# Kernel tuning notes

Measured on AMD Instinct MI355X. Metric: run time of the kernel, lower is better.

## Reference

```python
import jax, jax.numpy as jnp
import numpy as np

N_NODES = 50000
N_EDGES = 1600000
IN_FEATS = 256
NUM_HEADS = 4
OUT_FEATS = 32
NEG_SLOPE = 0.2


def setup_inputs() -> dict:
    key = jax.random.key(0)
    k_feat, k_src, k_dst, k_w, k_al, k_ar = jax.random.split(key, 6)
    feat = jax.random.normal(k_feat, (N_NODES, IN_FEATS), dtype=jnp.float32)
    src = jax.random.randint(k_src, (N_EDGES,), 0, N_NODES, dtype=jnp.int32)
    dst = jax.random.randint(k_dst, (N_EDGES,), 0, N_NODES, dtype=jnp.int32)
    # Glorot/xavier-like scales
    w_scale = np.sqrt(2.0 / (IN_FEATS + NUM_HEADS * OUT_FEATS)).astype(np.float32)
    a_scale = np.sqrt(2.0 / (1 + OUT_FEATS)).astype(np.float32)
    W_fc = jax.random.normal(k_w, (NUM_HEADS * OUT_FEATS, IN_FEATS), dtype=jnp.float32) * w_scale
    attn_l = jax.random.normal(k_al, (1, NUM_HEADS, OUT_FEATS), dtype=jnp.float32) * a_scale
    attn_r = jax.random.normal(k_ar, (1, NUM_HEADS, OUT_FEATS), dtype=jnp.float32) * a_scale
    bias = jnp.zeros((NUM_HEADS * OUT_FEATS,), dtype=jnp.float32)
    return {"feat": feat, "W_fc": W_fc, "attn_l": attn_l, "attn_r": attn_r,
            "bias": bias, "src": src, "dst": dst}


def reference(feat, W_fc, attn_l, attn_r, bias, src, dst):
    N = feat.shape[0]
    H, F = NUM_HEADS, OUT_FEATS
    # dense projection: [N, H, F]
    h = (feat @ W_fc.T).reshape(N, H, F)
    # per-node attention logits: [N, H]
    el = (h * attn_l).sum(axis=-1)
    er = (h * attn_r).sum(axis=-1)
    # u_add_v edge score + leaky relu: [E, H]
    e = el[src] + er[dst]
    e = jnp.where(e >= 0, e, NEG_SLOPE * e)
    # segment softmax over destination nodes
    m = jax.ops.segment_max(e, dst, num_segments=N)          # [N, H]
    m = jnp.where(jnp.isfinite(m), m, 0.0)                   # guard 0-in-degree
    e_exp = jnp.exp(e - m[dst])                              # [E, H]
    denom = jax.ops.segment_sum(e_exp, dst, num_segments=N)  # [N, H]
    denom = jnp.where(denom > 0, denom, 1.0)
    a = e_exp / denom[dst]                                   # [E, H]
    # weighted message aggregation: [N, H, F]
    msg = h[src] * a[:, :, None]                             # [E, H, F]
    out = jax.ops.segment_sum(msg, dst, num_segments=N)
    out = out + bias.reshape(1, H, F)
    return out
```

## Files before the change

kernel.cpp:

```cpp
#include <hip/hip_runtime.h>

typedef __attribute__((ext_vector_type(8))) short bf16x8;
typedef __attribute__((ext_vector_type(4))) float f32x4;

#define IN_F 256
#define HF 128
#define NHEADS 4
#define NEG 0.2f
#define GBM 128
#define GBK 64
#define LDK 72

#define RB 256
#define NBP 200
#define CHUNK 6400
#define ITPT 25
#define BCAP 10000

#define FUSED_SMEM (GBM * LDK * 2 * 2)

__device__ __forceinline__ unsigned short f2bf(float x) {
    unsigned u = __float_as_uint(x);
    unsigned r = (u + 0x7FFFu + ((u >> 16) & 1u)) >> 16;
    return (unsigned short)r;
}
__device__ __forceinline__ float bf2f(unsigned short b) {
    return __uint_as_float((unsigned)b << 16);
}

__global__ __launch_bounds__(256) void fused1_kernel(
    const float* __restrict__ feat, const float* __restrict__ W,
    const float* __restrict__ al, const float* __restrict__ ar,
    unsigned short* __restrict__ hb, float* __restrict__ el, float* __restrict__ er,
    const int* __restrict__ src, const int* __restrict__ dst,
    int* __restrict__ ebuf, int* __restrict__ cntArr, int* __restrict__ ofsArr,
    int N, int E, int GG)
{
    extern __shared__ char smem[];
    const int t = threadIdx.x;

    if ((int)blockIdx.x < GG) {
        unsigned short (*As)[LDK] = (unsigned short(*)[LDK])smem;
        unsigned short (*Bs)[LDK] = (unsigned short(*)[LDK])(smem + GBM * LDK * 2);
        const int n0 = blockIdx.x * GBM;
        const int lane = t & 63;
        const int wid = t >> 6;
        const int wm = (wid >> 1) * 64;
        const int wn = (wid & 1) * 64;
        const int lr = lane & 15;
        const int lk = (lane >> 4) * 8;

        f32x4 acc[4][4];
#pragma unroll
        for (int i = 0; i < 4; i++)
#pragma unroll
            for (int j = 0; j < 4; j++) acc[i][j] = (f32x4){0.f, 0.f, 0.f, 0.f};

        for (int k0 = 0; k0 < IN_F; k0 += GBK) {
#pragma unroll
            for (int r = 0; r < 4; r++) {
                int idx = t + r * 256;
                int row = idx >> 3;
                int c8 = (idx & 7) * 8;
                int n = n0 + row;
                float4 v0 = make_float4(0.f, 0.f, 0.f, 0.f), v1 = v0;
                if (n < N) {
                    v0 = *(const float4*)&feat[(size_t)n * IN_F + k0 + c8];
                    v1 = *(const float4*)&feat[(size_t)n * IN_F + k0 + c8 + 4];
                }
                bf16x8 sa;
                sa[0] = f2bf(v0.x); sa[1] = f2bf(v0.y); sa[2] = f2bf(v0.z); sa[3] = f2bf(v0.w);
                sa[4] = f2bf(v1.x); sa[5] = f2bf(v1.y); sa[6] = f2bf(v1.z); sa[7] = f2bf(v1.w);
                *(bf16x8*)&As[row][c8] = sa;
                float4 w0 = *(const float4*)&W[(size_t)row * IN_F + k0 + c8];
                float4 w1 = *(const float4*)&W[(size_t)row * IN_F + k0 + c8 + 4];
                bf16x8 sb;
                sb[0] = f2bf(w0.x); sb[1] = f2bf(w0.y); sb[2] = f2bf(w0.z); sb[3] = f2bf(w0.w);
                sb[4] = f2bf(w1.x); sb[5] = f2bf(w1.y); sb[6] = f2bf(w1.z); sb[7] = f2bf(w1.w);
                *(bf16x8*)&Bs[row][c8] = sb;
            }
            __syncthreads();
#pragma unroll
            for (int ks = 0; ks < 2; ks++) {
                bf16x8 a[4], b[4];
#pragma unroll
                for (int mi = 0; mi < 4; mi++) a[mi] = *(bf16x8*)&As[wm + mi * 16 + lr][ks * 32 + lk];
#pragma unroll
                for (int ni = 0; ni < 4; ni++) b[ni] = *(bf16x8*)&Bs[wn + ni * 16 + lr][ks * 32 + lk];
#pragma unroll
                for (int mi = 0; mi < 4; mi++)
#pragma unroll
                    for (int ni = 0; ni < 4; ni++)
                        acc[mi][ni] = __builtin_amdgcn_mfma_f32_16x16x32_bf16(a[mi], b[ni], acc[mi][ni], 0, 0, 0);
            }
            __syncthreads();
        }
        const int crow = (lane >> 4) * 4;
#pragma unroll
        for (int mi = 0; mi < 4; mi++)
#pragma unroll
            for (int j = 0; j < 4; j++) {
                int n = n0 + wm + mi * 16 + crow + j;
                if (n < N) {
#pragma unroll
                    for (int ni = 0; ni < 4; ni++) {
                        int o = wn + ni * 16 + lr;
                        hb[(size_t)n * HF + o] = f2bf(acc[mi][ni][j]);
                    }
                }
            }
        float al_c[4], ar_c[4];
#pragma unroll
        for (int ni = 0; ni < 4; ni++) {
            int o = wn + ni * 16 + lr;
            al_c[ni] = al[o];
            ar_c[ni] = ar[o];
        }
        float* elp = (float*)smem;
        float* erp = elp + 128 * 4;
        const int h0 = wn >> 5;
#pragma unroll
        for (int mi = 0; mi < 4; mi++)
#pragma unroll
            for (int j = 0; j < 4; j++) {
                float e0 = acc[mi][0][j] * al_c[0] + acc[mi][1][j] * al_c[1];
                float e1 = acc[mi][2][j] * al_c[2] + acc[mi][3][j] * al_c[3];
                float r0 = acc[mi][0][j] * ar_c[0] + acc[mi][1][j] * ar_c[1];
                float r1 = acc[mi][2][j] * ar_c[2] + acc[mi][3][j] * ar_c[3];
#pragma unroll
                for (int off = 1; off < 16; off <<= 1) {
                    e0 += __shfl_xor(e0, off);
                    e1 += __shfl_xor(e1, off);
                    r0 += __shfl_xor(r0, off);
                    r1 += __shfl_xor(r1, off);
                }
                if (lr == 0) {
                    int row = wm + mi * 16 + crow + j;
                    elp[row * 4 + h0]     = e0;
                    elp[row * 4 + h0 + 1] = e1;
                    erp[row * 4 + h0]     = r0;
                    erp[row * 4 + h0 + 1] = r1;
                }
            }
        __syncthreads();
        if (t < 128) {
            int n = n0 + t;
            if (n < N) {
                *(float4*)&el[(size_t)n * 4] = *(float4*)&elp[t * 4];
                *(float4*)&er[(size_t)n * 4] = *(float4*)&erp[t * 4];
            }
        }
    } else {
        int* cnt = (int*)smem;
        int* sc  = cnt + 256;
        int* cur = sc + 256;
        int* stage = cur + 256;
        const int blk = blockIdx.x - GG;
        const int eb = blk * CHUNK;
        cnt[t] = 0;
        __syncthreads();

        int bkt[ITPT], ent[ITPT];
#pragma unroll
        for (int i = 0; i < ITPT; i++) {
            int idx = eb + i * 256 + t;
            int b = NBP - 1, e = 0;
            if (idx < E) {
                int d = dst[idx];
                int s = src[idx];
                b = d >> 8;
                e = s | ((d & 255) << 24);
            }
            bkt[i] = b;
            ent[i] = e;
            atomicAdd(&cnt[b], 1);
        }
        __syncthreads();
        int orig = cnt[t];
        sc[t] = orig;
        __syncthreads();
        for (int off = 1; off < 256; off <<= 1) {
            int v = (t >= off) ? sc[t - off] : 0;
            __syncthreads();
            sc[t] += v;
            __syncthreads();
        }
        int excl = sc[t] - orig;
        if (t < NBP) {
            cntArr[blk * NBP + t] = orig;
            ofsArr[blk * NBP + t] = excl;
        }
        cur[t] = excl;
        __syncthreads();
#pragma unroll
        for (int i = 0; i < ITPT; i++) {
            int pos = atomicAdd(&cur[bkt[i]], 1);
            stage[pos] = ent[i];
        }
        __syncthreads();
#pragma unroll
        for (int i = 0; i < ITPT; i++) {
            int idx = i * 256 + t;
            ebuf[eb + idx] = stage[idx];
        }
    }
}

__global__ __launch_bounds__(256) void bscan_kernel(const int* __restrict__ cntArr,
                                                    int* __restrict__ bucketStart, int nblk) {
    __shared__ int sums[256];
    const int t = threadIdx.x;
    int s = 0;
    if (t < NBP)
        for (int blk = 0; blk < nblk; blk++) s += cntArr[blk * NBP + t];
    sums[t] = s;
    __syncthreads();
    for (int off = 1; off < 256; off <<= 1) {
        int v = (t >= off) ? sums[t - off] : 0;
        __syncthreads();
        sums[t] += v;
        __syncthreads();
    }
    if (t < NBP) bucketStart[t] = sums[t] - s;
}

__global__ __launch_bounds__(256) void bsort_kernel(const int* __restrict__ ebuf,
                                                    const int* __restrict__ cntArr,
                                                    const int* __restrict__ ofsArr,
                                                    const int* __restrict__ bucketStart,
                                                    int* __restrict__ rowStart,
                                                    int* __restrict__ esrc,
                                                    int nblk, int N, int E) {
    __shared__ int lcnt[256];
    __shared__ int lsc[256];
    __shared__ int lcur[256];
    __shared__ int sorted[BCAP];
    const int b = blockIdx.x, t = threadIdx.x;
    const int gbase = bucketStart[b];
    lcnt[t] = 0;
    __syncthreads();

    int rbase = 0, rlen = 0;
    if (t < nblk) {
        rbase = t * CHUNK + ofsArr[t * NBP + b];
        rlen = cntArr[t * NBP + b];
    }
    int i = 0;
    for (; i + 3 < rlen; i += 4) {
        unsigned e0 = (unsigned)ebuf[rbase + i];
        unsigned e1 = (unsigned)ebuf[rbase + i + 1];
        unsigned e2 = (unsigned)ebuf[rbase + i + 2];
        unsigned e3 = (unsigned)ebuf[rbase + i + 3];
        atomicAdd(&lcnt[e0 >> 24], 1);
        atomicAdd(&lcnt[e1 >> 24], 1);
        atomicAdd(&lcnt[e2 >> 24], 1);
        atomicAdd(&lcnt[e3 >> 24], 1);
    }
    for (; i < rlen; i++) {
        unsigned e = (unsigned)ebuf[rbase + i];
        atomicAdd(&lcnt[e >> 24], 1);
    }
    __syncthreads();
    int orig = lcnt[t];
    lsc[t] = orig;
    __syncthreads();
    for (int off = 1; off < 256; off <<= 1) {
        int v = (t >= off) ? lsc[t - off] : 0;
        __syncthreads();
        lsc[t] += v;
        __syncthreads();
    }
    int excl = lsc[t] - orig;
    int node = b * RB + t;
    if (node < N) rowStart[node] = gbase + excl;
    if (b == 0 && t == 0) rowStart[N] = E;
    lcur[t] = excl;
    __syncthreads();
    i = 0;
    for (; i + 3 < rlen; i += 4) {
        unsigned e0 = (unsigned)ebuf[rbase + i];
        unsigned e1 = (unsigned)ebuf[rbase + i + 1];
        unsigned e2 = (unsigned)ebuf[rbase + i + 2];
        unsigned e3 = (unsigned)ebuf[rbase + i + 3];
        sorted[atomicAdd(&lcur[e0 >> 24], 1)] = (int)(e0 & 0xFFFFFFu);
        sorted[atomicAdd(&lcur[e1 >> 24], 1)] = (int)(e1 & 0xFFFFFFu);
        sorted[atomicAdd(&lcur[e2 >> 24], 1)] = (int)(e2 & 0xFFFFFFu);
        sorted[atomicAdd(&lcur[e3 >> 24], 1)] = (int)(e3 & 0xFFFFFFu);
    }
    for (; i < rlen; i++) {
        unsigned e = (unsigned)ebuf[rbase + i];
        sorted[atomicAdd(&lcur[e >> 24], 1)] = (int)(e & 0xFFFFFFu);
    }
    __syncthreads();
    const int total = lsc[255];
    for (int k = t; k < total; k += 256) esrc[gbase + k] = sorted[k];
}

__global__ __launch_bounds__(256) void agg_kernel(const int* __restrict__ rowStart,
                                                  const int* __restrict__ esrc,
                                                  const unsigned short* __restrict__ hb,
                                                  const float* __restrict__ el,
                                                  const float* __restrict__ er,
                                                  const float* __restrict__ bias,
                                                  float* __restrict__ out, int N) {
    const int wid = threadIdx.x >> 6;
    const int lane = threadIdx.x & 63;
    const int n = blockIdx.x * 4 + wid;
    if (n >= N) return;
    const int lg = lane & 15;
    const int grp = lane >> 4;
    const int head = lg >> 2;
    const float ern = er[n * NHEADS + head];
    const int beg = rowStart[n];
    const int end = rowStart[n + 1];

    float acc[8];
#pragma unroll
    for (int i = 0; i < 8; i++) acc[i] = 0.f;
    float den = 0.f;

#pragma unroll 2
    for (int j = beg + grp; j < end; j += 4) {
        int s = esrc[j];
        float x = el[s * NHEADS + head] + ern;
        x = x >= 0.f ? x : NEG * x;
        float sv = __expf(x);
        uint4 hv = *(const uint4*)&hb[(size_t)s * HF + lg * 8];
        acc[0] += sv * bf2f((unsigned short)(hv.x & 0xFFFFu));
        acc[1] += sv * bf2f((unsigned short)(hv.x >> 16));
        acc[2] += sv * bf2f((unsigned short)(hv.y & 0xFFFFu));
        acc[3] += sv * bf2f((unsigned short)(hv.y >> 16));
        acc[4] += sv * bf2f((unsigned short)(hv.z & 0xFFFFu));
        acc[5] += sv * bf2f((unsigned short)(hv.z >> 16));
        acc[6] += sv * bf2f((unsigned short)(hv.w & 0xFFFFu));
        acc[7] += sv * bf2f((unsigned short)(hv.w >> 16));
        den += sv;
    }

#pragma unroll
    for (int off = 16; off < 64; off <<= 1) {
#pragma unroll
        for (int i = 0; i < 8; i++) acc[i] += __shfl_xor(acc[i], off);
        den += __shfl_xor(den, off);
    }

    if (lane < 16) {
        float inv = 1.f / (den > 0.f ? den : 1.f);
        float4 b0 = *(const float4*)&bias[lg * 8];
        float4 b1 = *(const float4*)&bias[lg * 8 + 4];
        float4 o0, o1;
        o0.x = acc[0] * inv + b0.x; o0.y = acc[1] * inv + b0.y;
        o0.z = acc[2] * inv + b0.z; o0.w = acc[3] * inv + b0.w;
        o1.x = acc[4] * inv + b1.x; o1.y = acc[5] * inv + b1.y;
        o1.z = acc[6] * inv + b1.z; o1.w = acc[7] * inv + b1.w;
        *(float4*)&out[(size_t)n * HF + lg * 8] = o0;
        *(float4*)&out[(size_t)n * HF + lg * 8 + 4] = o1;
    }
}

extern "C" void kernel_launch(void* const* d_in, const int* in_sizes, int n_in,
                              void* d_out, int out_size, void* d_ws, size_t ws_size,
                              hipStream_t stream) {
    const float* feat = (const float*)d_in[0];
    const float* W    = (const float*)d_in[1];
    const float* al   = (const float*)d_in[2];
    const float* ar   = (const float*)d_in[3];
    const float* bias = (const float*)d_in[4];
    const int*   src  = (const int*)d_in[5];
    const int*   dst  = (const int*)d_in[6];
    const int N = in_sizes[0] / IN_F;
    const int E = in_sizes[5];
    float* out = (float*)d_out;

    const int nblk = (E + CHUNK - 1) / CHUNK;
    const int NBUCK = (N + RB - 1) / RB;
    const int GG = (N + GBM - 1) / GBM;

    unsigned short* hb = (unsigned short*)d_ws;
    float* el       = (float*)(hb + (size_t)N * HF);
    float* er       = el + (size_t)N * NHEADS;
    int* rowStart   = (int*)(er + (size_t)N * NHEADS);
    int* esrc       = rowStart + (N + 1);
    int* ebuf       = esrc + E;
    int* cntArr     = ebuf + (size_t)nblk * CHUNK;
    int* ofsArr     = cntArr + (size_t)nblk * NBP;
    int* bucketStart= ofsArr + (size_t)nblk * NBP;

    fused1_kernel<<<GG + nblk, 256, FUSED_SMEM, stream>>>(
        feat, W, al, ar, hb, el, er, src, dst, ebuf, cntArr, ofsArr, N, E, GG);
    bscan_kernel<<<1, 256, 0, stream>>>(cntArr, bucketStart, nblk);
    bsort_kernel<<<NBUCK, 256, 0, stream>>>(ebuf, cntArr, ofsArr, bucketStart,
                                            rowStart, esrc, nblk, N, E);
    agg_kernel<<<(N + 3) / 4, 256, 0, stream>>>(rowStart, esrc, hb, el, er, bias, out, N);
}
```

Measured before the change: 140.9 us.

## Pre-convert W to bf16 and compute GEMM directly from registers without LDS

Adds a small kernel that converts W to bf16 once per call. The projection GEMM then drops its LDS staging and barriers: each wave loads its 32 feature rows straight from global into MFMA operands and reads the bf16 W fragments from global/L2. Each wave now covers all 128 output columns, so el/er are reduced inside the wave and written directly. The cost is an extra launch and redundant W reads per wave, which rely on cache hits. The shared-memory size is also set from the partition branch's needs.

Measured after the change: 163.8 us. 1.16x slower.

```diff
diff --git a/kernel.cpp b/kernel.cpp
--- a/kernel.cpp
+++ b/kernel.cpp
@@ -7,9 +7,6 @@
 #define HF 128
 #define NHEADS 4
 #define NEG 0.2f
-#define GBM 128
-#define GBK 64
-#define LDK 72
 
 #define RB 256
 #define NBP 200
@@ -17,7 +14,7 @@
 #define ITPT 25
 #define BCAP 10000
 
-#define FUSED_SMEM (GBM * LDK * 2 * 2)
+#define PART_SMEM ((256 * 3 + CHUNK) * 4)
 
 __device__ __forceinline__ unsigned short f2bf(float x) {
     unsigned u = __float_as_uint(x);
@@ -27,9 +24,26 @@
 __device__ __forceinline__ float bf2f(unsigned short b) {
     return __uint_as_float((unsigned)b << 16);
 }
+__device__ __forceinline__ bf16x8 cvt8(float4 x, float4 y) {
+    bf16x8 r;
+    r[0] = f2bf(x.x); r[1] = f2bf(x.y); r[2] = f2bf(x.z); r[3] = f2bf(x.w);
+    r[4] = f2bf(y.x); r[5] = f2bf(y.y); r[6] = f2bf(y.z); r[7] = f2bf(y.w);
+    return r;
+}
+
+__global__ __launch_bounds__(256) void wconv_kernel(const float* __restrict__ W,
+                                                    unsigned short* __restrict__ Wb) {
+    int i = (blockIdx.x * 256 + threadIdx.x) * 4;
+    if (i < HF * IN_F) {
+        float4 v = *(const float4*)&W[i];
+        ushort4 o;
+        o.x = f2bf(v.x); o.y = f2bf(v.y); o.z = f2bf(v.z); o.w = f2bf(v.w);
+        *(ushort4*)&Wb[i] = o;
+    }
+}
 
 __global__ __launch_bounds__(256) void fused1_kernel(
-    const float* __restrict__ feat, const float* __restrict__ W,
+    const float* __restrict__ feat, const unsigned short* __restrict__ Wb,
     const float* __restrict__ al, const float* __restrict__ ar,
     unsigned short* __restrict__ hb, float* __restrict__ el, float* __restrict__ er,
     const int* __restrict__ src, const int* __restrict__ dst,
@@ -40,116 +54,84 @@
     const int t = threadIdx.x;
 
     if ((int)blockIdx.x < GG) {
-        unsigned short (*As)[LDK] = (unsigned short(*)[LDK])smem;
-        unsigned short (*Bs)[LDK] = (unsigned short(*)[LDK])(smem + GBM * LDK * 2);
-        const int n0 = blockIdx.x * GBM;
         const int lane = t & 63;
         const int wid = t >> 6;
-        const int wm = (wid >> 1) * 64;
-        const int wn = (wid & 1) * 64;
+        const int base = blockIdx.x * 128 + wid * 32;
         const int lr = lane & 15;
-        const int lk = (lane >> 4) * 8;
-
-        f32x4 acc[4][4];
-#pragma unroll
-        for (int i = 0; i < 4; i++)
-#pragma unroll
-            for (int j = 0; j < 4; j++) acc[i][j] = (f32x4){0.f, 0.f, 0.f, 0.f};
-
-        for (int k0 = 0; k0 < IN_F; k0 += GBK) {
-#pragma unroll
-            for (int r = 0; r < 4; r++) {
-                int idx = t + r * 256;
-                int row = idx >> 3;
-                int c8 = (idx & 7) * 8;
-                int n = n0 + row;
-                float4 v0 = make_float4(0.f, 0.f, 0.f, 0.f), v1 = v0;
+        const int lkO = (lane >> 4) * 8;
+
+        const int r0 = base + lr;
+        const int r1 = base + 16 + lr;
+        const bool v0 = r0 < N, v1 = r1 < N;
+        const float* arow0 = feat + (size_t)r0 * IN_F + lkO;
+        const float* arow1 = feat + (size_t)r1 * IN_F + lkO;
+
+        f32x4 acc[2][8];
+#pragma unroll
+        for (int mi = 0; mi < 2; mi++)
+#pragma unroll
+            for (int ni = 0; ni < 8; ni++) acc[mi][ni] = (f32x4){0.f, 0.f, 0.f, 0.f};
+
+        const float4 z4 = make_float4(0.f, 0.f, 0.f, 0.f);
+#pragma unroll
+        for (int ks = 0; ks < 8; ks++) {
+            const int k0 = ks * 32;
+            bf16x8 a0, a1;
+            {
+                float4 x0 = v0 ? *(const float4*)(arow0 + k0) : z4;
+                float4 x1 = v0 ? *(const float4*)(arow0 + k0 + 4) : z4;
+                a0 = cvt8(x0, x1);
+                float4 y0 = v1 ? *(const float4*)(arow1 + k0) : z4;
+                float4 y1 = v1 ? *(const float4*)(arow1 + k0 + 4) : z4;
+                a1 = cvt8(y0, y1);
+            }
+            bf16x8 b[8];
+#pragma unroll
+            for (int ni = 0; ni < 8; ni++)
+                b[ni] = *(const bf16x8*)&Wb[(size_t)(ni * 16 + lr) * IN_F + k0 + lkO];
+#pragma unroll
+            for (int ni = 0; ni < 8; ni++) {
+                acc[0][ni] = __builtin_amdgcn_mfma_f32_16x16x32_bf16(a0, b[ni], acc[0][ni], 0, 0, 0);
+                acc[1][ni] = __builtin_amdgcn_mfma_f32_16x16x32_bf16(a1, b[ni], acc[1][ni], 0, 0, 0);
+            }
+        }
+
+        float al_c[8], ar_c[8];
+#pragma unroll
+        for (int ni = 0; ni < 8; ni++) {
+            al_c[ni] = al[ni * 16 + lr];
+            ar_c[ni] = ar[ni * 16 + lr];
+        }
+        const int crow = (lane >> 4) * 4;
+#pragma unroll
+        for (int mi = 0; mi < 2; mi++)
+#pragma unroll
+            for (int j = 0; j < 4; j++) {
+                int n = base + mi * 16 + crow + j;
                 if (n < N) {
-                    v0 = *(const float4*)&feat[(size_t)n * IN_F + k0 + c8];
-                    v1 = *(const float4*)&feat[(size_t)n * IN_F + k0 + c8 + 4];
+#pragma unroll
+                    for (int ni = 0; ni < 8; ni++)
+                        hb[(size_t)n * HF + ni * 16 + lr] = f2bf(acc[mi][ni][j]);
                 }
-                bf16x8 sa;
-                sa[0] = f2bf(v0.x); sa[1] = f2bf(v0.y); sa[2] = f2bf(v0.z); sa[3] = f2bf(v0.w);
-                sa[4] = f2bf(v1.x); sa[5] = f2bf(v1.y); sa[6] = f2bf(v1.z); sa[7] = f2bf(v1.w);
-                *(bf16x8*)&As[row][c8] = sa;
-                float4 w0 = *(const float4*)&W[(size_t)row * IN_F + k0 + c8];
-                float4 w1 = *(const float4*)&W[(size_t)row * IN_F + k0 + c8 + 4];
-                bf16x8 sb;
-                sb[0] = f2bf(w0.x); sb[1] = f2bf(w0.y); sb[2] = f2bf(w0.z); sb[3] = f2bf(w0.w);
-                sb[4] = f2bf(w1.x); sb[5] = f2bf(w1.y); sb[6] = f2bf(w1.z); sb[7] = f2bf(w1.w);
-                *(bf16x8*)&Bs[row][c8] = sb;
-            }
-            __syncthreads();
-#pragma unroll
-            for (int ks = 0; ks < 2; ks++) {
-                bf16x8 a[4], b[4];
-#pragma unroll
-                for (int mi = 0; mi < 4; mi++) a[mi] = *(bf16x8*)&As[wm + mi * 16 + lr][ks * 32 + lk];
-#pragma unroll
-                for (int ni = 0; ni < 4; ni++) b[ni] = *(bf16x8*)&Bs[wn + ni * 16 + lr][ks * 32 + lk];
-#pragma unroll
-                for (int mi = 0; mi < 4; mi++)
-#pragma unroll
-                    for (int ni = 0; ni < 4; ni++)
-                        acc[mi][ni] = __builtin_amdgcn_mfma_f32_16x16x32_bf16(a[mi], b[ni], acc[mi][ni], 0, 0, 0);
-            }
-            __syncthreads();
-        }
-        const int crow = (lane >> 4) * 4;
-#pragma unroll
-        for (int mi = 0; mi < 4; mi++)
-#pragma unroll
-            for (int j = 0; j < 4; j++) {
-                int n = n0 + wm + mi * 16 + crow + j;
-                if (n < N) {
-#pragma unroll
-                    for (int ni = 0; ni < 4; ni++) {
-                        int o = wn + ni * 16 + lr;
-                        hb[(size_t)n * HF + o] = f2bf(acc[mi][ni][j]);
+                float e[4], r[4];
+#pragma unroll
+                for (int h = 0; h < 4; h++) {
+                    e[h] = acc[mi][2 * h][j] * al_c[2 * h] + acc[mi][2 * h + 1][j] * al_c[2 * h + 1];
+                    r[h] = acc[mi][2 * h][j] * ar_c[2 * h] + acc[mi][2 * h + 1][j] * ar_c[2 * h + 1];
+                }
+#pragma unroll
+                for (int off = 1; off < 16; off <<= 1) {
+#pragma unroll
+                    for (int h = 0; h < 4; h++) {
+                        e[h] += __shfl_xor(e[h], off);
+                        r[h] += __shfl_xor(r[h], off);
                     }
                 }
-            }
-        float al_c[4], ar_c[4];
-#pragma unroll
-        for (int ni = 0; ni < 4; ni++) {
-            int o = wn + ni * 16 + lr;
-            al_c[ni] = al[o];
-            ar_c[ni] = ar[o];
-        }
-        float* elp = (float*)smem;
-        float* erp = elp + 128 * 4;
-        const int h0 = wn >> 5;
-#pragma unroll
-        for (int mi = 0; mi < 4; mi++)
-#pragma unroll
-            for (int j = 0; j < 4; j++) {
-                float e0 = acc[mi][0][j] * al_c[0] + acc[mi][1][j] * al_c[1];
-                float e1 = acc[mi][2][j] * al_c[2] + acc[mi][3][j] * al_c[3];
-                float r0 = acc[mi][0][j] * ar_c[0] + acc[mi][1][j] * ar_c[1];
-                float r1 = acc[mi][2][j] * ar_c[2] + acc[mi][3][j] * ar_c[3];
-#pragma unroll
-                for (int off = 1; off < 16; off <<= 1) {
-                    e0 += __shfl_xor(e0, off);
-                    e1 += __shfl_xor(e1, off);
-                    r0 += __shfl_xor(r0, off);
-                    r1 += __shfl_xor(r1, off);
-                }
-                if (lr == 0) {
-                    int row = wm + mi * 16 + crow + j;
-                    elp[row * 4 + h0]     = e0;
-                    elp[row * 4 + h0 + 1] = e1;
-                    erp[row * 4 + h0]     = r0;
-                    erp[row * 4 + h0 + 1] = r1;
+                if (lr == 0 && n < N) {
+                    *(float4*)&el[(size_t)n * 4] = make_float4(e[0], e[1], e[2], e[3]);
+                    *(float4*)&er[(size_t)n * 4] = make_float4(r[0], r[1], r[2], r[3]);
                 }
             }
-        __syncthreads();
-        if (t < 128) {
-            int n = n0 + t;
-            if (n < N) {
-                *(float4*)&el[(size_t)n * 4] = *(float4*)&elp[t * 4];
-                *(float4*)&er[(size_t)n * 4] = *(float4*)&erp[t * 4];
-            }
-        }
     } else {
         int* cnt = (int*)smem;
         int* sc  = cnt + 256;
@@ -374,10 +356,11 @@
 
     const int nblk = (E + CHUNK - 1) / CHUNK;
     const int NBUCK = (N + RB - 1) / RB;
-    const int GG = (N + GBM - 1) / GBM;
+    const int GG = (N + 127) / 128;
 
     unsigned short* hb = (unsigned short*)d_ws;
-    float* el       = (float*)(hb + (size_t)N * HF);
+    unsigned short* Wb = hb + (size_t)N * HF;
+    float* el       = (float*)(Wb + HF * IN_F);
     float* er       = el + (size_t)N * NHEADS;
     int* rowStart   = (int*)(er + (size_t)N * NHEADS);
     int* esrc       = rowStart + (N + 1);
@@ -386,8 +369,9 @@
     int* ofsArr     = cntArr + (size_t)nblk * NBP;
     int* bucketStart= ofsArr + (size_t)nblk * NBP;
 
-    fused1_kernel<<<GG + nblk, 256, FUSED_SMEM, stream>>>(
-        feat, W, al, ar, hb, el, er, src, dst, ebuf, cntArr, ofsArr, N, E, GG);
+    wconv_kernel<<<(HF * IN_F / 4 + 255) / 256, 256, 0, stream>>>(W, Wb);
+    fused1_kernel<<<GG + nblk, 256, PART_SMEM, stream>>>(
+        feat, Wb, al, ar, hb, el, er, src, dst, ebuf, cntArr, ofsArr, N, E, GG);
     bscan_kernel<<<1, 256, 0, stream>>>(cntArr, bucketStart, nblk);
     bsort_kernel<<<NBUCK, 256, 0, stream>>>(ebuf, cntArr, ofsArr, bucketStart,
                                             rowStart, esrc, nblk, N, E);
```
